# Kernel optimization log

Measured on AMD Instinct MI355X. Metric: run time of the kernel, lower is better.

## Reference

```python
import jax, jax.numpy as jnp
import numpy as np

B, S, D, U, WIN = 32, 4096, 1024, 1024, 64


def setup_inputs() -> dict:
    key = jax.random.key(0)
    k1, k2, k3, k4, k5 = jax.random.split(key, 5)
    query = jax.random.normal(k1, (B, D), dtype=jnp.float32)
    keys = jax.random.normal(k2, (B, S, D), dtype=jnp.float32)
    key_lengths = jax.random.randint(k3, (B,), S // 2, S).astype(jnp.float32)
    Wq = jax.random.normal(k4, (D, U), dtype=jnp.float32) / np.sqrt(D)
    wp = jax.random.normal(k5, (U, 1), dtype=jnp.float32) / np.sqrt(U)
    return {"query": query, "keys": keys, "key_lengths": key_lengths,
            "Wq": Wq, "wp": wp, "window_size": WIN}


def reference(query, keys, key_lengths, Wq, wp, window_size):
    # dot score: [B,1,D] @ [B,D,S] -> [B,S]
    alignment_score = jnp.einsum('bd,bsd->bs', query, keys)
    weight = jax.nn.softmax(alignment_score, axis=-1)  # F.softmax on 2D -> dim 1

    kl = key_lengths[:, None]                                   # [B,1]
    activated_query = jnp.tanh(query @ Wq)                      # [B,U]
    sigmoid_query = jax.nn.sigmoid(activated_query @ wp)        # [B,1]
    predictive_alignment = kl * sigmoid_query                   # [B,1]

    std2 = jnp.float32((window_size / 2.0) ** 2)
    dist = (kl - predictive_alignment) ** 2                     # [B,1]
    gauss = jnp.exp(-dist / (2.0 * std2))                       # [B,1]

    weight = weight * gauss                                     # [B,S]
    total_context = jnp.einsum('bs,bsd->bd', weight, keys)      # [B,D]
    return total_context, alignment_score
```

## Files before the change

kernel.cpp:

```cpp
#include <hip/hip_runtime.h>
#include <math.h>

#define BB 32
#define SS 4096
#define DD 1024
#define UU 1024
#define TROWS 4
#define CHROWS 128
#define NT (CHROWS / TROWS)
#define CHB (SS / CHROWS)
#define FBLK (BB * CHB)
#define GBLK 128
#define NPART CHB

#define LOAD_LDS16(g, l) __builtin_amdgcn_global_load_lds( \
    (const __attribute__((address_space(1))) unsigned int*)(g), \
    (__attribute__((address_space(3))) unsigned int*)(l), 16, 0, 0)

#define STAGE(ti, dst) do {                                              \
    const char* gt_ = gbase + (size_t)(ti) * 16384;                      \
    char* lb_ = (char*)smem + (dst) * 16384;                             \
    _Pragma("unroll")                                                    \
    for (int j_ = 0; j_ < 4; ++j_)                                       \
        LOAD_LDS16(gt_ + j_ * 4096 + tid * 16, lb_ + j_ * 4096 + tid * 16); \
} while (0)


__global__ __launch_bounds__(256, 3) void fused_kernel(const float* __restrict__ query,
                                                       const float* __restrict__ keys,
                                                       const float* __restrict__ Wq,
                                                       const float* __restrict__ wp,
                                                       float* __restrict__ scores,
                                                       float* __restrict__ mlbuf,
                                                       float* __restrict__ accbuf,
                                                       float* __restrict__ gpart) {
    __shared__ float smem[12288];

    if (blockIdx.x < GBLK) {
        int g = blockIdx.x;
        int u0 = g * 8;
        float4* s4 = (float4*)smem;
        for (int i = threadIdx.x; i < 2048; i += 256) {
            int d = i >> 1, h = i & 1;
            s4[i] = *(const float4*)(Wq + (size_t)d * UU + u0 + h * 4);
        }
        __syncthreads();
        int b = threadIdx.x >> 3, ui = threadIdx.x & 7;
        const float* qb = query + (size_t)b * DD;
        float acc = 0.f;
#pragma unroll 8
        for (int d = 0; d < DD; ++d) acc += qb[d] * smem[d * 8 + ui];
        float val = tanhf(acc) * wp[u0 + ui];
        val += __shfl_xor(val, 1, 64);
        val += __shfl_xor(val, 2, 64);
        val += __shfl_xor(val, 4, 64);
        if (ui == 0) gpart[b * GBLK + g] = val;
        return;
    }

    int fb = blockIdx.x - GBLK;
    int b = fb >> 5;
    int chunk = fb & (CHB - 1);
    int s0 = chunk * CHROWS;
    int w = threadIdx.x >> 6;
    int lane = threadIdx.x & 63;
    int tid = threadIdx.x;

    const float4* Q4 = (const float4*)query;
    float4 q0 = Q4[b * 256 + lane],       q1 = Q4[b * 256 + lane + 64],
           q2 = Q4[b * 256 + lane + 128], q3 = Q4[b * 256 + lane + 192];

    const char* gbase = (const char*)(keys + ((size_t)b * SS + s0) * DD);
    float4 a0 = {0,0,0,0}, a1 = {0,0,0,0}, a2 = {0,0,0,0}, a3 = {0,0,0,0};
    float m = -INFINITY, l = 0.f;

    STAGE(0, 0);
    STAGE(1, 1);

    int bf = 0;
    for (int t = 0; t < NT; ++t) {
        if (t + 1 < NT) {
            asm volatile("s_waitcnt vmcnt(4)" ::: "memory");
        } else {
            asm volatile("s_waitcnt vmcnt(0)" ::: "memory");
        }
        __builtin_amdgcn_s_barrier();

        if (t + 2 < NT) {
            int nb = bf + 2; if (nb >= 3) nb -= 3;
            STAGE(t + 2, nb);
        }

        const float* rowp = smem + bf * 4096 + w * 1024;
        float4 k0 = *(const float4*)(rowp + (lane)       * 4);
        float4 k1 = *(const float4*)(rowp + (lane + 64)  * 4);
        float4 k2 = *(const float4*)(rowp + (lane + 128) * 4);
        float4 k3 = *(const float4*)(rowp + (lane + 192) * 4);

        float d = k0.x*q0.x + k0.y*q0.y + k0.z*q0.z + k0.w*q0.w
                + k1.x*q1.x + k1.y*q1.y + k1.z*q1.z + k1.w*q1.w
                + k2.x*q2.x + k2.y*q2.y + k2.z*q2.z + k2.w*q2.w
                + k3.x*q3.x + k3.y*q3.y + k3.z*q3.z + k3.w*q3.w;
#pragma unroll
        for (int o = 32; o > 0; o >>= 1) d += __shfl_xor(d, o, 64);

        if (lane == 0) scores[(size_t)b * SS + s0 + t * TROWS + w] = d;

        float mn = fmaxf(m, d);
        float corr = __expf(m - mn);
        float p = __expf(d - mn);
        l = l * corr + p;
        a0.x = a0.x*corr + p*k0.x; a0.y = a0.y*corr + p*k0.y; a0.z = a0.z*corr + p*k0.z; a0.w = a0.w*corr + p*k0.w;
        a1.x = a1.x*corr + p*k1.x; a1.y = a1.y*corr + p*k1.y; a1.z = a1.z*corr + p*k1.z; a1.w = a1.w*corr + p*k1.w;
        a2.x = a2.x*corr + p*k2.x; a2.y = a2.y*corr + p*k2.y; a2.z = a2.z*corr + p*k2.z; a2.w = a2.w*corr + p*k2.w;
        a3.x = a3.x*corr + p*k3.x; a3.y = a3.y*corr + p*k3.y; a3.z = a3.z*corr + p*k3.z; a3.w = a3.w*corr + p*k3.w;
        m = mn;

        bf += 1; if (bf >= 3) bf -= 3;
    }

    __syncthreads();
    if (lane == 0) { smem[8192 + w] = m; smem[8196 + w] = l; }
    __syncthreads();
    float M = fmaxf(fmaxf(smem[8192], smem[8193]), fmaxf(smem[8194], smem[8195]));
    float Ls = smem[8196] * __expf(smem[8192] - M) + smem[8197] * __expf(smem[8193] - M)
             + smem[8198] * __expf(smem[8194] - M) + smem[8199] * __expf(smem[8195] - M);
    float sw = __expf(m - M);
    float4* aw = (float4*)(smem + (size_t)w * 1024);
    float4 t0 = {a0.x*sw, a0.y*sw, a0.z*sw, a0.w*sw};
    float4 t1 = {a1.x*sw, a1.y*sw, a1.z*sw, a1.w*sw};
    float4 t2 = {a2.x*sw, a2.y*sw, a2.z*sw, a2.w*sw};
    float4 t3 = {a3.x*sw, a3.y*sw, a3.z*sw, a3.w*sw};
    __syncthreads();
    aw[lane] = t0; aw[lane + 64] = t1; aw[lane + 128] = t2; aw[lane + 192] = t3;
    __syncthreads();
    float4 s = {0,0,0,0};
#pragma unroll
    for (int w2 = 0; w2 < 4; ++w2) {
        float4 v = ((const float4*)(smem + (size_t)w2 * 1024))[tid];
        s.x += v.x; s.y += v.y; s.z += v.z; s.w += v.w;
    }
    ((float4*)(accbuf + (size_t)fb * DD))[tid] = s;
    if (tid == 0) { mlbuf[fb * 2] = M; mlbuf[fb * 2 + 1] = Ls; }
}

__global__ void combine_kernel(const float* __restrict__ mlbuf,
                               const float* __restrict__ accbuf,
                               const float* __restrict__ gpart,
                               const float* __restrict__ key_lengths,
                               const int* __restrict__ win,
                               float* __restrict__ ctx) {
    int b = blockIdx.x;
    int d = blockIdx.y * 256 + threadIdx.x;

    __shared__ float red[128];
    __shared__ float mv[NPART], lv[NPART], wexp[NPART];

    if (threadIdx.x < 128) red[threadIdx.x] = gpart[b * GBLK + threadIdx.x];
    if (threadIdx.x < NPART) {
        mv[threadIdx.x] = mlbuf[(b * NPART + threadIdx.x) * 2];
        lv[threadIdx.x] = mlbuf[(b * NPART + threadIdx.x) * 2 + 1];
    }
    __syncthreads();
    for (int t = 64; t > 0; t >>= 1) {
        if (threadIdx.x < t) red[threadIdx.x] += red[threadIdx.x + t];
        __syncthreads();
    }
    float presig = red[0];

    float M = -INFINITY;
#pragma unroll
    for (int i = 0; i < NPART; ++i) M = fmaxf(M, mv[i]);
    float L = 0.f;
#pragma unroll
    for (int i = 0; i < NPART; ++i) L += lv[i] * __expf(mv[i] - M);
    __syncthreads();
    if (threadIdx.x < NPART) wexp[threadIdx.x] = __expf(mv[threadIdx.x] - M);
    __syncthreads();

    float acc = 0.f;
#pragma unroll 8
    for (int i = 0; i < NPART; ++i)
        acc += wexp[i] * accbuf[((size_t)b * NPART + i) * DD + d];

    float sig = 1.f / (1.f + __expf(-presig));
    float kl = key_lengths[b];
    float pa = kl * sig;
    float wv = (float)(*win);
    float std2 = (wv * 0.5f) * (wv * 0.5f);
    float g = __expf(-((kl - pa) * (kl - pa)) / (2.f * std2));

    ctx[(size_t)b * DD + d] = acc * g / L;
}

extern "C" void kernel_launch(void* const* d_in, const int* in_sizes, int n_in,
                              void* d_out, int out_size, void* d_ws, size_t ws_size,
                              hipStream_t stream) {
    const float* query       = (const float*)d_in[0];
    const float* keys        = (const float*)d_in[1];
    const float* key_lengths = (const float*)d_in[2];
    const float* Wq          = (const float*)d_in[3];
    const float* wp          = (const float*)d_in[4];
    const int*   win         = (const int*)d_in[5];

    float* out    = (float*)d_out;
    float* ctx    = out;
    float* scores = out + BB * DD;
    float* wsbuf  = (float*)d_ws;
    float* gpart  = wsbuf;
    float* mlbuf  = wsbuf + 4096;
    float* accbuf = wsbuf + 8192;

    fused_kernel<<<FBLK + GBLK, 256, 0, stream>>>(query, keys, Wq, wp,
                                                  scores, mlbuf, accbuf, gpart);

    dim3 cgrid(BB, DD / 256);
    combine_kernel<<<cgrid, 256, 0, stream>>>(mlbuf, accbuf, gpart, key_lengths, win, ctx);
}
```

Baseline: 113.4 us.

## Give each wave its own contiguous rows and private LDS ring, dropping block barriers

Each wave now owns 32 contiguous key rows of the block's chunk. It streams them through its own three-slot LDS ring with per-wave async global-to-LDS loads, so the per-row block-wide s_barrier goes away. The dot product is split into four partial sums to shorten the dependency chain. The risk is ordering: with no barrier, each lane relies only on its own vmcnt wait before reading LDS that other lanes wrote. That may be unsafe, and the per-wave 4 KB streams are less coalesced across the block than before.

```diff
diff --git a/kernel.cpp b/kernel.cpp
--- a/kernel.cpp
+++ b/kernel.cpp
@@ -5,9 +5,8 @@
 #define SS 4096
 #define DD 1024
 #define UU 1024
-#define TROWS 4
+#define WROWS 32
 #define CHROWS 128
-#define NT (CHROWS / TROWS)
 #define CHB (SS / CHROWS)
 #define FBLK (BB * CHB)
 #define GBLK 128
@@ -17,12 +16,12 @@
     (const __attribute__((address_space(1))) unsigned int*)(g), \
     (__attribute__((address_space(3))) unsigned int*)(l), 16, 0, 0)
 
-#define STAGE(ti, dst) do {                                              \
-    const char* gt_ = gbase + (size_t)(ti) * 16384;                      \
-    char* lb_ = (char*)smem + (dst) * 16384;                             \
+#define STAGE_W(ti, dst) do {                                            \
+    const char* gt_ = gwave + (size_t)(ti) * 4096;                       \
+    char* lb_ = wbase + (dst) * 4096;                                    \
     _Pragma("unroll")                                                    \
     for (int j_ = 0; j_ < 4; ++j_)                                       \
-        LOAD_LDS16(gt_ + j_ * 4096 + tid * 16, lb_ + j_ * 4096 + tid * 16); \
+        LOAD_LDS16(gt_ + j_ * 1024 + lane * 16, lb_ + j_ * 1024 + lane * 16); \
 } while (0)
 
 
@@ -70,41 +69,43 @@
     float4 q0 = Q4[b * 256 + lane],       q1 = Q4[b * 256 + lane + 64],
            q2 = Q4[b * 256 + lane + 128], q3 = Q4[b * 256 + lane + 192];
 
-    const char* gbase = (const char*)(keys + ((size_t)b * SS + s0) * DD);
+    const char* gwave = (const char*)(keys + ((size_t)b * SS + s0 + w * WROWS) * DD);
+    char* wbase = (char*)smem + w * 12288;
+    size_t scorebase = (size_t)b * SS + s0 + w * WROWS;
+
     float4 a0 = {0,0,0,0}, a1 = {0,0,0,0}, a2 = {0,0,0,0}, a3 = {0,0,0,0};
     float m = -INFINITY, l = 0.f;
 
-    STAGE(0, 0);
-    STAGE(1, 1);
+    STAGE_W(0, 0);
+    STAGE_W(1, 1);
 
     int bf = 0;
-    for (int t = 0; t < NT; ++t) {
-        if (t + 1 < NT) {
+    for (int t = 0; t < WROWS; ++t) {
+        if (t + 1 < WROWS) {
             asm volatile("s_waitcnt vmcnt(4)" ::: "memory");
         } else {
             asm volatile("s_waitcnt vmcnt(0)" ::: "memory");
         }
-        __builtin_amdgcn_s_barrier();
-
-        if (t + 2 < NT) {
+        if (t + 2 < WROWS) {
             int nb = bf + 2; if (nb >= 3) nb -= 3;
-            STAGE(t + 2, nb);
+            STAGE_W(t + 2, nb);
         }
 
-        const float* rowp = smem + bf * 4096 + w * 1024;
+        const float* rowp = (const float*)(wbase + bf * 4096);
         float4 k0 = *(const float4*)(rowp + (lane)       * 4);
         float4 k1 = *(const float4*)(rowp + (lane + 64)  * 4);
         float4 k2 = *(const float4*)(rowp + (lane + 128) * 4);
         float4 k3 = *(const float4*)(rowp + (lane + 192) * 4);
 
-        float d = k0.x*q0.x + k0.y*q0.y + k0.z*q0.z + k0.w*q0.w
-                + k1.x*q1.x + k1.y*q1.y + k1.z*q1.z + k1.w*q1.w
-                + k2.x*q2.x + k2.y*q2.y + k2.z*q2.z + k2.w*q2.w
-                + k3.x*q3.x + k3.y*q3.y + k3.z*q3.z + k3.w*q3.w;
+        float d0 = k0.x*q0.x + k0.y*q0.y + k0.z*q0.z + k0.w*q0.w;
+        float d1 = k1.x*q1.x + k1.y*q1.y + k1.z*q1.z + k1.w*q1.w;
+        float d2 = k2.x*q2.x + k2.y*q2.y + k2.z*q2.z + k2.w*q2.w;
+        float d3 = k3.x*q3.x + k3.y*q3.y + k3.z*q3.z + k3.w*q3.w;
+        float d = (d0 + d1) + (d2 + d3);
 #pragma unroll
         for (int o = 32; o > 0; o >>= 1) d += __shfl_xor(d, o, 64);
 
-        if (lane == 0) scores[(size_t)b * SS + s0 + t * TROWS + w] = d;
+        if (lane == 0) scores[scorebase + t] = d;
 
         float mn = fmaxf(m, d);
         float corr = __expf(m - mn);
```

Measured after the change: 126.7 us. +11.6%, slower.

## Fuse combine stage into main kernel via last-block atomic counters

Applied to the files above, without the earlier changes.

Removes the separate combine kernel launch. Each block increments a per-batch atomic counter after a threadfence, and the last block to arrive for a batch performs the split-softmax combine and gating for that batch. This saves a kernel launch and its dependency gap. In exchange it adds a memset launch, atomics, and a serialized combine tail done by one block per batch instead of four.

```diff
diff --git a/kernel.cpp b/kernel.cpp
--- a/kernel.cpp
+++ b/kernel.cpp
@@ -12,6 +12,7 @@
 #define FBLK (BB * CHB)
 #define GBLK 128
 #define NPART CHB
+#define TARGET (CHB + GBLK)
 
 #define LOAD_LDS16(g, l) __builtin_amdgcn_global_load_lds( \
     (const __attribute__((address_space(1))) unsigned int*)(g), \
@@ -26,26 +27,76 @@
 } while (0)
 
 
+__device__ __forceinline__ void combine_b(int b, float* smem,
+                                          const float* mlbuf, const float* accbuf,
+                                          const float* gpart, const float* key_lengths,
+                                          const int* win, float* ctx, int tid) {
+    float* cm = smem;
+    if (tid < 32) {
+        cm[tid]      = mlbuf[(b * NPART + tid) * 2];
+        cm[32 + tid] = mlbuf[(b * NPART + tid) * 2 + 1];
+    }
+    if (tid >= 64 && tid < 192) cm[tid] = gpart[b * GBLK + (tid - 64)];
+    __syncthreads();
+    for (int t = 64; t > 0; t >>= 1) {
+        if (tid < t) cm[64 + tid] += cm[64 + tid + t];
+        __syncthreads();
+    }
+    float presig = cm[64];
+    float M = -INFINITY;
+#pragma unroll
+    for (int i = 0; i < 32; ++i) M = fmaxf(M, cm[i]);
+    float L = 0.f;
+#pragma unroll
+    for (int i = 0; i < 32; ++i) L += cm[32 + i] * __expf(cm[i] - M);
+    if (tid < 32) cm[192 + tid] = __expf(cm[tid] - M);
+    __syncthreads();
+
+    float sig = 1.f / (1.f + __expf(-presig));
+    float kl = key_lengths[b];
+    float pa = kl * sig;
+    float wv = (float)(*win);
+    float std2 = (wv * 0.5f) * (wv * 0.5f);
+    float g = __expf(-((kl - pa) * (kl - pa)) / (2.f * std2)) / L;
+
+    const float4* ab = (const float4*)accbuf + (size_t)b * NPART * 256;
+    float4 acc = {0.f, 0.f, 0.f, 0.f};
+#pragma unroll 8
+    for (int i = 0; i < NPART; ++i) {
+        float4 v = ab[(size_t)i * 256 + tid];
+        float we = cm[192 + i];
+        acc.x += we * v.x; acc.y += we * v.y; acc.z += we * v.z; acc.w += we * v.w;
+    }
+    float4 o = {acc.x * g, acc.y * g, acc.z * g, acc.w * g};
+    ((float4*)ctx)[b * 256 + tid] = o;
+}
+
 __global__ __launch_bounds__(256, 3) void fused_kernel(const float* __restrict__ query,
                                                        const float* __restrict__ keys,
                                                        const float* __restrict__ Wq,
                                                        const float* __restrict__ wp,
+                                                       const float* __restrict__ key_lengths,
+                                                       const int* __restrict__ win,
                                                        float* __restrict__ scores,
                                                        float* __restrict__ mlbuf,
                                                        float* __restrict__ accbuf,
-                                                       float* __restrict__ gpart) {
+                                                       float* __restrict__ gpart,
+                                                       int* __restrict__ cnt,
+                                                       float* __restrict__ ctx) {
     __shared__ float smem[12288];
+
+    int tid = threadIdx.x;
 
     if (blockIdx.x < GBLK) {
         int g = blockIdx.x;
         int u0 = g * 8;
         float4* s4 = (float4*)smem;
-        for (int i = threadIdx.x; i < 2048; i += 256) {
+        for (int i = tid; i < 2048; i += 256) {
             int d = i >> 1, h = i & 1;
             s4[i] = *(const float4*)(Wq + (size_t)d * UU + u0 + h * 4);
         }
         __syncthreads();
-        int b = threadIdx.x >> 3, ui = threadIdx.x & 7;
+        int b = tid >> 3, ui = tid & 7;
         const float* qb = query + (size_t)b * DD;
         float acc = 0.f;
 #pragma unroll 8
@@ -55,6 +106,26 @@
         val += __shfl_xor(val, 2, 64);
         val += __shfl_xor(val, 4, 64);
         if (ui == 0) gpart[b * GBLK + g] = val;
+
+        __threadfence();
+        __syncthreads();
+        if (tid == 0) {
+            unsigned mask = 0;
+            for (int b2 = 0; b2 < BB; ++b2) {
+                int old = atomicAdd(&cnt[b2], 1);
+                if (old == TARGET - 1) mask |= 1u << b2;
+            }
+            ((unsigned*)smem)[0] = mask;
+        }
+        __syncthreads();
+        unsigned mask = ((unsigned*)smem)[0];
+        __syncthreads();
+        while (mask) {
+            int b2 = __ffs(mask) - 1;
+            mask &= mask - 1;
+            combine_b(b2, smem, mlbuf, accbuf, gpart, key_lengths, win, ctx, tid);
+            __syncthreads();
+        }
         return;
     }
 
@@ -62,9 +133,8 @@
     int b = fb >> 5;
     int chunk = fb & (CHB - 1);
     int s0 = chunk * CHROWS;
-    int w = threadIdx.x >> 6;
-    int lane = threadIdx.x & 63;
-    int tid = threadIdx.x;
+    int w = tid >> 6;
+    int lane = tid & 63;
 
     const float4* Q4 = (const float4*)query;
     float4 q0 = Q4[b * 256 + lane],       q1 = Q4[b * 256 + lane + 64],
@@ -142,55 +212,17 @@
     }
     ((float4*)(accbuf + (size_t)fb * DD))[tid] = s;
     if (tid == 0) { mlbuf[fb * 2] = M; mlbuf[fb * 2 + 1] = Ls; }
-}
-
-__global__ void combine_kernel(const float* __restrict__ mlbuf,
-                               const float* __restrict__ accbuf,
-                               const float* __restrict__ gpart,
-                               const float* __restrict__ key_lengths,
-                               const int* __restrict__ win,
-                               float* __restrict__ ctx) {
-    int b = blockIdx.x;
-    int d = blockIdx.y * 256 + threadIdx.x;
-
-    __shared__ float red[128];
-    __shared__ float mv[NPART], lv[NPART], wexp[NPART];
-
-    if (threadIdx.x < 128) red[threadIdx.x] = gpart[b * GBLK + threadIdx.x];
-    if (threadIdx.x < NPART) {
-        mv[threadIdx.x] = mlbuf[(b * NPART + threadIdx.x) * 2];
-        lv[threadIdx.x] = mlbuf[(b * NPART + threadIdx.x) * 2 + 1];
-    }
-    __syncthreads();
-    for (int t = 64; t > 0; t >>= 1) {
-        if (threadIdx.x < t) red[threadIdx.x] += red[threadIdx.x + t];
-        __syncthreads();
-    }
-    float presig = red[0];
-
-    float M = -INFINITY;
-#pragma unroll
-    for (int i = 0; i < NPART; ++i) M = fmaxf(M, mv[i]);
-    float L = 0.f;
-#pragma unroll
-    for (int i = 0; i < NPART; ++i) L += lv[i] * __expf(mv[i] - M);
-    __syncthreads();
-    if (threadIdx.x < NPART) wexp[threadIdx.x] = __expf(mv[threadIdx.x] - M);
-    __syncthreads();
-
-    float acc = 0.f;
-#pragma unroll 8
-    for (int i = 0; i < NPART; ++i)
-        acc += wexp[i] * accbuf[((size_t)b * NPART + i) * DD + d];
-
-    float sig = 1.f / (1.f + __expf(-presig));
-    float kl = key_lengths[b];
-    float pa = kl * sig;
-    float wv = (float)(*win);
-    float std2 = (wv * 0.5f) * (wv * 0.5f);
-    float g = __expf(-((kl - pa) * (kl - pa)) / (2.f * std2));
-
-    ctx[(size_t)b * DD + d] = acc * g / L;
+
+    __threadfence();
+    __syncthreads();
+    if (tid == 0) {
+        int old = atomicAdd(&cnt[b], 1);
+        ((int*)smem)[0] = (old == TARGET - 1) ? 1 : 0;
+    }
+    __syncthreads();
+    int doit = ((int*)smem)[0];
+    __syncthreads();
+    if (doit) combine_b(b, smem, mlbuf, accbuf, gpart, key_lengths, win, ctx, tid);
 }
 
 extern "C" void kernel_launch(void* const* d_in, const int* in_sizes, int n_in,
@@ -209,11 +241,11 @@
     float* wsbuf  = (float*)d_ws;
     float* gpart  = wsbuf;
     float* mlbuf  = wsbuf + 4096;
+    int*   cnt    = (int*)(wsbuf + 6144);
     float* accbuf = wsbuf + 8192;
 
-    fused_kernel<<<FBLK + GBLK, 256, 0, stream>>>(query, keys, Wq, wp,
-                                                  scores, mlbuf, accbuf, gpart);
-
-    dim3 cgrid(BB, DD / 256);
-    combine_kernel<<<cgrid, 256, 0, stream>>>(mlbuf, accbuf, gpart, key_lengths, win, ctx);
+    hipMemsetAsync(cnt, 0, BB * sizeof(int), stream);
+
+    fused_kernel<<<FBLK + GBLK, 256, 0, stream>>>(query, keys, Wq, wp, key_lengths, win,
+                                                  scores, mlbuf, accbuf, gpart, cnt, ctx);
 }
```

After: 370.4 us. +226.5%, slower.
